# Performance work log

Hardware: AMD Instinct MI355X
Metric: run time of the kernel (lower is better)

## Reference

```python
import jax, jax.numpy as jnp
import numpy as np

N = 1024
X_DIM = 256
Y_DIM = 256
HIDDEN = 256


def setup_inputs() -> dict:
    key = jax.random.key(0)
    ks = jax.random.split(key, 6)
    lim1 = 1.0 / np.sqrt(X_DIM + Y_DIM)
    lim2 = 1.0 / np.sqrt(HIDDEN)
    return {
        "x_samples": jax.random.normal(ks[0], (N, X_DIM), jnp.float32),
        "y_samples": jax.random.normal(ks[1], (N, Y_DIM), jnp.float32),
        # F_func params: Linear(x_dim+y_dim, hidden) -> ReLU -> Linear(hidden, 1)
        "W1": jax.random.uniform(ks[2], (X_DIM + Y_DIM, HIDDEN), jnp.float32, -lim1, lim1),
        "b1": jax.random.uniform(ks[3], (HIDDEN,), jnp.float32, -lim1, lim1),
        "W2": jax.random.uniform(ks[4], (HIDDEN, 1), jnp.float32, -lim2, lim2),
        "b2": jax.random.uniform(ks[5], (1,), jnp.float32, -lim2, lim2),
    }


def reference(x_samples, y_samples, W1, b1, W2, b2):
    n = y_samples.shape[0]
    # Diagonal (joint) term: F([x_i, y_i])
    t0 = jnp.maximum(jnp.concatenate([x_samples, y_samples], axis=-1) @ W1 + b1, 0.0) @ W2 + b2  # [N,1]
    # Pairwise term: decompose first Linear into x- and y-projections, broadcast-sum.
    px = x_samples @ W1[:X_DIM]   # [N, H]
    py = y_samples @ W1[X_DIM:]   # [N, H]
    # torch layout: row axis = y tile, col axis = x tile -> h[i, j] = relu(py_i + px_j + b1)
    h = jnp.maximum(py[:, None, :] + px[None, :, :] + b1, 0.0)          # [N, N, H]
    t1 = jnp.einsum("yxh,ho->yx", h, W2) + b2[0] - 1.0                   # [N, N]
    # logsumexp over dim=1 (x axis), then exp-mean
    lse = jax.nn.logsumexp(t1, axis=1) - jnp.log(jnp.float32(n))         # [N]
    lower_bound = t0.mean() - jnp.exp(lse).mean()
    return lower_bound
```

## Files before the change

kernel.cpp:

```cpp
#include <hip/hip_runtime.h>

#define NS 1024
#define KD 256
#define H  256
#define PAIR_NBLK 512

#define GLOAD_LDS16(gp, lp)                                                         \
    __builtin_amdgcn_global_load_lds(                                               \
        (const __attribute__((address_space(1))) void*)(gp),                        \
        (__attribute__((address_space(3))) void*)(lp), 16, 0, 0)

__global__ __launch_bounds__(256) void proj_kernel(
    const float* __restrict__ X, const float* __restrict__ Y,
    const float* __restrict__ W1, const float* __restrict__ b1,
    const float* __restrict__ W2,
    float* __restrict__ PXT, float* __restrict__ PYT,
    float* __restrict__ FX, float* __restrict__ GY)
{
    const int z = blockIdx.z;
    const float* __restrict__ A = z ? Y : X;
    const float* __restrict__ W = W1 + (z ? (size_t)KD * H : 0);
    float* __restrict__ OUT = z ? PYT : PXT;
    float* __restrict__ RS  = z ? GY : FX;

    __shared__ float xs[KD][34];
    __shared__ float fred[8][33];

    const int tid = threadIdx.x;
    const int jl = tid & 31;
    const int hg = tid >> 5;
    const int i0 = blockIdx.y * 32, h0 = blockIdx.x * 32;

    {
        const int ii = tid & 31, q = tid >> 5;
        #pragma unroll
        for (int u = 0; u < 8; ++u) {
            const int k = u * 32 + q * 4;
            float4 v = *(const float4*)&A[(i0 + ii) * KD + k];
            xs[k + 0][ii] = v.x; xs[k + 1][ii] = v.y;
            xs[k + 2][ii] = v.z; xs[k + 3][ii] = v.w;
        }
    }
    __syncthreads();

    float acc[4] = {};
    const float* __restrict__ wp = &W[h0 + hg * 4];
    #pragma unroll 8
    for (int k = 0; k < KD; ++k) {
        float4 w4 = *(const float4*)&wp[(size_t)k * H];
        const float xv = xs[k][jl];
        acc[0] = fmaf(xv, w4.x, acc[0]);
        acc[1] = fmaf(xv, w4.y, acc[1]);
        acc[2] = fmaf(xv, w4.z, acc[2]);
        acc[3] = fmaf(xv, w4.w, acc[3]);
    }

    if (z) {
        float4 bv = *(const float4*)&b1[h0 + hg * 4];
        acc[0] += bv.x; acc[1] += bv.y; acc[2] += bv.z; acc[3] += bv.w;
    }

    float4 w2v = *(const float4*)&W2[h0 + hg * 4];
    float fp = 0.f;
    const float w2a[4] = {w2v.x, w2v.y, w2v.z, w2v.w};
    #pragma unroll
    for (int c = 0; c < 4; ++c) {
        const int h = h0 + hg * 4 + c;
        OUT[(size_t)h * NS + i0 + jl] = acc[c];
        fp = fmaf(w2a[c], acc[c], fp);
    }
    fred[hg][jl] = fp;
    __syncthreads();
    if (tid < 32) {
        float s = 0.f;
        #pragma unroll
        for (int g = 0; g < 8; ++g) s += fred[g][tid];
        atomicAdd(&RS[i0 + tid], s);
    }
}

__global__ __launch_bounds__(256) void pair_kernel(
    const float* __restrict__ PXT, const float* __restrict__ PYT,
    const float* __restrict__ W2, const float* __restrict__ b2,
    const float* __restrict__ FX, const float* __restrict__ GY,
    float* __restrict__ eparts, float* __restrict__ dparts,
    int* __restrict__ counter, float* __restrict__ out)
{
    __shared__ float pxs[2][32][128];
    __shared__ float pys[256][16];
    __shared__ float w2s[H];
    __shared__ float red_e[256], red_d[256];
    __shared__ double sde[256], sdd[256];
    __shared__ int lastflag;

    const int tid = threadIdx.x;
    const int lane = tid & 63;
    const int wid = __builtin_amdgcn_readfirstlane(tid >> 6);
    const int j0 = blockIdx.x * 128;
    const int i0 = blockIdx.y * 16;

#define STAGE(T, B)                                                             \
    {                                                                           \
        const float* gb = &PXT[(size_t)((T) * 32) * NS + j0];                   \
        _Pragma("unroll")                                                       \
        for (int p = 0; p < 4; ++p) {                                           \
            const int hrow = 8 * p + 2 * wid + (lane >> 5);                     \
            const float* g = gb + (size_t)hrow * NS + (lane & 31) * 4;          \
            float* l = &pxs[B][hrow][(lane & 31) * 4];                          \
            GLOAD_LDS16(g, l);                                                  \
        }                                                                       \
    }

    STAGE(0, 0);

    {
        const int ii = tid & 15, hb = tid >> 4;
        #pragma unroll
        for (int u = 0; u < 16; ++u) {
            const int h = hb * 16 + u;
            pys[h][ii] = PYT[(size_t)h * NS + i0 + ii];
        }
        w2s[tid] = W2[tid];
    }
    __syncthreads();

    float acc[4][2] = {};

    for (int T = 0; T < 8; ++T) {
        const int B = T & 1;
        if (T < 7) STAGE(T + 1, B ^ 1);
        #pragma unroll
        for (int hh = 0; hh < 32; ++hh) {
            const int hT = T * 32 + hh;
            float2 px2 = *(const float2*)&pxs[B][hh][lane * 2];
            float4 p4  = *(const float4*)&pys[hT][wid * 4];
            const float w = w2s[hT];
            const float pya[4] = {p4.x, p4.y, p4.z, p4.w};
            #pragma unroll
            for (int r = 0; r < 4; ++r) {
                acc[r][0] = fmaf(fabsf(pya[r] + px2.x), w, acc[r][0]);
                acc[r][1] = fmaf(fabsf(pya[r] + px2.y), w, acc[r][1]);
            }
        }
        __syncthreads();
    }

    const float c0 = b2[0] - 1.0f;
    float2 fx2 = *(const float2*)&FX[j0 + lane * 2];
    float4 g4 = *(const float4*)&GY[i0 + wid * 4];
    const float gya[4] = {g4.x, g4.y, g4.z, g4.w};
    const float fxa[2] = {fx2.x, fx2.y};

    float esum = 0.f, dsum = 0.f;
    #pragma unroll
    for (int r = 0; r < 4; ++r) {
        const int irow = i0 + wid * 4 + r;
        #pragma unroll
        for (int c = 0; c < 2; ++c) {
            const float t1 = fmaf(0.5f, acc[r][c] + gya[r] + fxa[c], c0);
            esum += expf(t1);
            if (irow == j0 + lane * 2 + c) dsum += t1 + 1.0f;
        }
    }

    red_e[tid] = esum;
    red_d[tid] = dsum;
    __syncthreads();
    for (int s = 128; s > 0; s >>= 1) {
        if (tid < s) {
            red_e[tid] += red_e[tid + s];
            red_d[tid] += red_d[tid + s];
        }
        __syncthreads();
    }

    const int bid = blockIdx.y * gridDim.x + blockIdx.x;
    if (tid == 0) {
        __hip_atomic_store(&eparts[bid], red_e[0], __ATOMIC_RELAXED, __HIP_MEMORY_SCOPE_AGENT);
        __hip_atomic_store(&dparts[bid], red_d[0], __ATOMIC_RELAXED, __HIP_MEMORY_SCOPE_AGENT);
        __threadfence();
        const int prev = __hip_atomic_fetch_add(counter, 1, __ATOMIC_ACQ_REL, __HIP_MEMORY_SCOPE_AGENT);
        lastflag = (prev == PAIR_NBLK - 1);
    }
    __syncthreads();

    if (lastflag) {
        __threadfence();
        sde[tid] = (double)__hip_atomic_load(&eparts[tid], __ATOMIC_RELAXED, __HIP_MEMORY_SCOPE_AGENT)
                 + (double)__hip_atomic_load(&eparts[tid + 256], __ATOMIC_RELAXED, __HIP_MEMORY_SCOPE_AGENT);
        sdd[tid] = (double)__hip_atomic_load(&dparts[tid], __ATOMIC_RELAXED, __HIP_MEMORY_SCOPE_AGENT)
                 + (double)__hip_atomic_load(&dparts[tid + 256], __ATOMIC_RELAXED, __HIP_MEMORY_SCOPE_AGENT);
        __syncthreads();
        for (int s = 128; s > 0; s >>= 1) {
            if (tid < s) { sde[tid] += sde[tid + s]; sdd[tid] += sdd[tid + s]; }
            __syncthreads();
        }
        if (tid == 0)
            out[0] = (float)(sdd[0] / (double)NS - sde[0] / ((double)NS * (double)NS));
    }
#undef STAGE
}

extern "C" void kernel_launch(void* const* d_in, const int* in_sizes, int n_in,
                              void* d_out, int out_size, void* d_ws, size_t ws_size,
                              hipStream_t stream)
{
    const float* X  = (const float*)d_in[0];
    const float* Y  = (const float*)d_in[1];
    const float* W1 = (const float*)d_in[2];
    const float* b1 = (const float*)d_in[3];
    const float* W2 = (const float*)d_in[4];
    const float* b2 = (const float*)d_in[5];
    float* out = (float*)d_out;

    float* PXT    = (float*)d_ws;
    float* PYT    = PXT + (size_t)H * NS;
    float* eparts = PYT + (size_t)H * NS;
    float* dparts = eparts + 512;
    float* FX     = dparts + 512;
    float* GY     = FX + NS;
    int*   counter = (int*)(GY + NS);

    hipMemsetAsync(FX, 0, (size_t)(2 * NS) * sizeof(float) + sizeof(int), stream);

    proj_kernel<<<dim3(8, 32, 2), 256, 0, stream>>>(X, Y, W1, b1, W2, PXT, PYT, FX, GY);
    pair_kernel<<<dim3(8, 64), 256, 0, stream>>>(PXT, PYT, W2, b2, FX, GY,
                                                 eparts, dparts, counter, out);
}
```

Measured before the change: 122.4 us.

## Fold |W2| into projections, sort hidden units by W2 sign, deepen pipeline

The projection kernel scales each projected hidden unit by |W2[h]| and permutes hidden rows so positive-weight units come first. This lets the pair kernel replace the per-cell fma with a plain add into separate positive and negative accumulators, subtracted at the end. The pair kernel also moves to a 4-buffer, 16-row staging pipeline with explicit vmcnt waits and raw barriers, loads PY via async LDS loads, and sets launch bounds for 2 blocks per SU. The changes add per-block ballot/prefix work, more accumulator registers, and a mixed-sign tile branch.

```diff
diff --git a/kernel.cpp b/kernel.cpp
--- a/kernel.cpp
+++ b/kernel.cpp
@@ -14,19 +14,38 @@
     const float* __restrict__ X, const float* __restrict__ Y,
     const float* __restrict__ W1, const float* __restrict__ b1,
     const float* __restrict__ W2,
-    float* __restrict__ PXT, float* __restrict__ PYT,
+    float* __restrict__ PXW, float* __restrict__ PYW,
     float* __restrict__ FX, float* __restrict__ GY)
 {
+    __shared__ float xs[KD][34];
+    __shared__ float fred[8][33];
+    __shared__ int dsts[H];
+    __shared__ int woff[4];
+
+    const int tid = threadIdx.x;
+
+    {
+        const float w = W2[tid];
+        const bool pos = (w >= 0.0f);
+        const unsigned long long m = __ballot(pos);
+        const int lane = tid & 63, wv = tid >> 6;
+        const int below = __popcll(m & ((1ull << lane) - 1ull));
+        if (lane == 0) woff[wv] = __popcll(m);
+        __syncthreads();
+        const int npos = woff[0] + woff[1] + woff[2] + woff[3];
+        int posbase = 0;
+        #pragma unroll
+        for (int q = 0; q < 4; ++q) if (q < wv) posbase += woff[q];
+        const int negbase = npos + (wv * 64 - posbase);
+        dsts[tid] = pos ? (posbase + below) : (negbase + ((tid & 63) - below));
+    }
+
     const int z = blockIdx.z;
     const float* __restrict__ A = z ? Y : X;
     const float* __restrict__ W = W1 + (z ? (size_t)KD * H : 0);
-    float* __restrict__ OUT = z ? PYT : PXT;
+    float* __restrict__ OUT = z ? PYW : PXW;
     float* __restrict__ RS  = z ? GY : FX;
 
-    __shared__ float xs[KD][34];
-    __shared__ float fred[8][33];
-
-    const int tid = threadIdx.x;
     const int jl = tid & 31;
     const int hg = tid >> 5;
     const int i0 = blockIdx.y * 32, h0 = blockIdx.x * 32;
@@ -61,12 +80,14 @@
     }
 
     float4 w2v = *(const float4*)&W2[h0 + hg * 4];
+    const float w2a[4] = {w2v.x, w2v.y, w2v.z, w2v.w};
+    int d4[4];
+    *(int4*)d4 = *(const int4*)&dsts[h0 + hg * 4];
+
     float fp = 0.f;
-    const float w2a[4] = {w2v.x, w2v.y, w2v.z, w2v.w};
     #pragma unroll
     for (int c = 0; c < 4; ++c) {
-        const int h = h0 + hg * 4 + c;
-        OUT[(size_t)h * NS + i0 + jl] = acc[c];
+        OUT[(size_t)d4[c] * NS + i0 + jl] = acc[c] * fabsf(w2a[c]);
         fp = fmaf(w2a[c], acc[c], fp);
     }
     fred[hg][jl] = fp;
@@ -79,18 +100,18 @@
     }
 }
 
-__global__ __launch_bounds__(256) void pair_kernel(
-    const float* __restrict__ PXT, const float* __restrict__ PYT,
+__global__ __launch_bounds__(256, 2) void pair_kernel(
+    const float* __restrict__ PXW, const float* __restrict__ PYW,
     const float* __restrict__ W2, const float* __restrict__ b2,
     const float* __restrict__ FX, const float* __restrict__ GY,
     float* __restrict__ eparts, float* __restrict__ dparts,
     int* __restrict__ counter, float* __restrict__ out)
 {
-    __shared__ float pxs[2][32][128];
+    __shared__ float pxs[4][16][128];
     __shared__ float pys[256][16];
-    __shared__ float w2s[H];
     __shared__ float red_e[256], red_d[256];
     __shared__ double sde[256], sdd[256];
+    __shared__ int wcnt[4];
     __shared__ int lastflag;
 
     const int tid = threadIdx.x;
@@ -99,50 +120,92 @@
     const int j0 = blockIdx.x * 128;
     const int i0 = blockIdx.y * 16;
 
-#define STAGE(T, B)                                                             \
+    {
+        const float w = W2[tid];
+        const unsigned long long m = __ballot(w >= 0.0f);
+        if (lane == 0) wcnt[wid] = __popcll(m);
+    }
+    __syncthreads();
+    const int Npos = __builtin_amdgcn_readfirstlane(wcnt[0] + wcnt[1] + wcnt[2] + wcnt[3]);
+
+    {
+        float* pysf = &pys[0][0];
+        #pragma unroll
+        for (int q = 0; q < 4; ++q) {
+            const int seg = wid * 4 + q;
+            const int h = seg * 16 + (lane >> 2);
+            const float* g = &PYW[(size_t)h * NS + i0 + (lane & 3) * 4];
+            GLOAD_LDS16(g, pysf + seg * 256 + lane * 4);
+        }
+    }
+
+#define STAGE(T)                                                                \
     {                                                                           \
-        const float* gb = &PXT[(size_t)((T) * 32) * NS + j0];                   \
+        const int _b = (T) & 3;                                                 \
         _Pragma("unroll")                                                       \
-        for (int p = 0; p < 4; ++p) {                                           \
-            const int hrow = 8 * p + 2 * wid + (lane >> 5);                     \
-            const float* g = gb + (size_t)hrow * NS + (lane & 31) * 4;          \
-            float* l = &pxs[B][hrow][(lane & 31) * 4];                          \
-            GLOAD_LDS16(g, l);                                                  \
+        for (int p = 0; p < 2; ++p) {                                           \
+            const int hrow = p * 8 + wid * 2 + (lane >> 5);                     \
+            const float* g = &PXW[(size_t)((T) * 16 + hrow) * NS + j0 + (lane & 31) * 4]; \
+            GLOAD_LDS16(g, &pxs[_b][hrow][(lane & 31) * 4]);                    \
         }                                                                       \
     }
 
-    STAGE(0, 0);
-
-    {
-        const int ii = tid & 15, hb = tid >> 4;
-        #pragma unroll
-        for (int u = 0; u < 16; ++u) {
-            const int h = hb * 16 + u;
-            pys[h][ii] = PYT[(size_t)h * NS + i0 + ii];
-        }
-        w2s[tid] = W2[tid];
-    }
-    __syncthreads();
-
-    float acc[4][2] = {};
-
-    for (int T = 0; T < 8; ++T) {
-        const int B = T & 1;
-        if (T < 7) STAGE(T + 1, B ^ 1);
-        #pragma unroll
-        for (int hh = 0; hh < 32; ++hh) {
-            const int hT = T * 32 + hh;
-            float2 px2 = *(const float2*)&pxs[B][hh][lane * 2];
-            float4 p4  = *(const float4*)&pys[hT][wid * 4];
-            const float w = w2s[hT];
-            const float pya[4] = {p4.x, p4.y, p4.z, p4.w};
+    STAGE(0); STAGE(1); STAGE(2);
+
+    float accP[4][2] = {}, accN[4][2] = {};
+
+#define CELLS(ACC)                                                              \
+    _Pragma("unroll")                                                           \
+    for (int hh = 0; hh < 16; ++hh) {                                           \
+        float2 px2 = *(const float2*)(pxb + hh * 128);                          \
+        float4 p4  = *(const float4*)(pyb + hh * 16);                           \
+        const float pya[4] = {p4.x, p4.y, p4.z, p4.w};                          \
+        _Pragma("unroll")                                                       \
+        for (int r = 0; r < 4; ++r) {                                           \
+            ACC[r][0] += fabsf(pya[r] + px2.x);                                 \
+            ACC[r][1] += fabsf(pya[r] + px2.y);                                 \
+        }                                                                       \
+    }
+
+    for (int T = 0; T < 16; ++T) {
+        if (T <= 13)      asm volatile("s_waitcnt vmcnt(4)" ::: "memory");
+        else if (T == 14) asm volatile("s_waitcnt vmcnt(2)" ::: "memory");
+        else              asm volatile("s_waitcnt vmcnt(0)" ::: "memory");
+        __builtin_amdgcn_sched_barrier(0);
+        __builtin_amdgcn_s_barrier();
+        __builtin_amdgcn_sched_barrier(0);
+
+        if (T < 13) STAGE(T + 3);
+
+        const int hbase = T * 16;
+        const float* pxb = &pxs[T & 3][0][lane * 2];
+        const float* pyb = &pys[hbase][wid * 4];
+
+        if (hbase + 16 <= Npos) {
+            CELLS(accP)
+        } else if (hbase >= Npos) {
+            CELLS(accN)
+        } else {
             #pragma unroll
-            for (int r = 0; r < 4; ++r) {
-                acc[r][0] = fmaf(fabsf(pya[r] + px2.x), w, acc[r][0]);
-                acc[r][1] = fmaf(fabsf(pya[r] + px2.y), w, acc[r][1]);
+            for (int hh = 0; hh < 16; ++hh) {
+                float2 px2 = *(const float2*)(pxb + hh * 128);
+                float4 p4  = *(const float4*)(pyb + hh * 16);
+                const float pya[4] = {p4.x, p4.y, p4.z, p4.w};
+                if (hbase + hh < Npos) {
+                    #pragma unroll
+                    for (int r = 0; r < 4; ++r) {
+                        accP[r][0] += fabsf(pya[r] + px2.x);
+                        accP[r][1] += fabsf(pya[r] + px2.y);
+                    }
+                } else {
+                    #pragma unroll
+                    for (int r = 0; r < 4; ++r) {
+                        accN[r][0] += fabsf(pya[r] + px2.x);
+                        accN[r][1] += fabsf(pya[r] + px2.y);
+                    }
+                }
             }
         }
-        __syncthreads();
     }
 
     const float c0 = b2[0] - 1.0f;
@@ -157,7 +220,8 @@
         const int irow = i0 + wid * 4 + r;
         #pragma unroll
         for (int c = 0; c < 2; ++c) {
-            const float t1 = fmaf(0.5f, acc[r][c] + gya[r] + fxa[c], c0);
+            const float A = accP[r][c] - accN[r][c];
+            const float t1 = fmaf(0.5f, A + gya[r] + fxa[c], c0);
             esum += expf(t1);
             if (irow == j0 + lane * 2 + c) dsum += t1 + 1.0f;
         }
@@ -199,6 +263,7 @@
             out[0] = (float)(sdd[0] / (double)NS - sde[0] / ((double)NS * (double)NS));
     }
 #undef STAGE
+#undef CELLS
 }
 
 extern "C" void kernel_launch(void* const* d_in, const int* in_sizes, int n_in,
@@ -213,9 +278,9 @@
     const float* b2 = (const float*)d_in[5];
     float* out = (float*)d_out;
 
-    float* PXT    = (float*)d_ws;
-    float* PYT    = PXT + (size_t)H * NS;
-    float* eparts = PYT + (size_t)H * NS;
+    float* PXW    = (float*)d_ws;
+    float* PYW    = PXW + (size_t)H * NS;
+    float* eparts = PYW + (size_t)H * NS;
     float* dparts = eparts + 512;
     float* FX     = dparts + 512;
     float* GY     = FX + NS;
@@ -223,7 +288,7 @@
 
     hipMemsetAsync(FX, 0, (size_t)(2 * NS) * sizeof(float) + sizeof(int), stream);
 
-    proj_kernel<<<dim3(8, 32, 2), 256, 0, stream>>>(X, Y, W1, b1, W2, PXT, PYT, FX, GY);
-    pair_kernel<<<dim3(8, 64), 256, 0, stream>>>(PXT, PYT, W2, b2, FX, GY,
+    proj_kernel<<<dim3(8, 32, 2), 256, 0, stream>>>(X, Y, W1, b1, W2, PXW, PYW, FX, GY);
+    pair_kernel<<<dim3(8, 64), 256, 0, stream>>>(PXW, PYW, W2, b2, FX, GY,
                                                  eparts, dparts, counter, out);
 }
```

After: 129.8 us. 6.1% more time.
